# Kernel tuning notes

Measured on AMD Instinct MI355X. Metric: run time of the kernel, lower is better.

## Reference

```python
import jax, jax.numpy as jnp
import numpy as np

B, T, D, C = 16, 2048, 512, 20
K_EASY, K_HARD = 40, 20
M_BIG, M_SMALL = 7, 3
A4 = A5 = A6 = A7 = 1.0
EPS = 1e-05
DROP_P = 0.6


def setup_inputs() -> dict:
    key = jax.random.key(0)
    ks = jax.random.split(key, 6)
    attn = jax.random.uniform(ks[0], (B, T, 1), dtype=jnp.float32)
    mu = jax.random.normal(ks[1], (B, T, D), dtype=jnp.float32)
    var = jax.random.uniform(ks[2], (B, T, D), dtype=jnp.float32) * 0.9 + 0.1
    mu_clip = jax.random.normal(ks[3], (B, T, D), dtype=jnp.float32)
    text_feat = jax.random.normal(ks[4], (C, D), dtype=jnp.float32)
    keep = (jax.random.uniform(ks[5], (B, T)) >= DROP_P).astype(jnp.float32)
    drop_mask = keep / (1.0 - DROP_P)  # inverted-dropout mask on a ones tensor
    return dict(attn=attn, mu=mu, var=var, mu_clip=mu_clip, text_feat=text_feat, drop_mask=drop_mask)


def _normalize(x, axis=-1):
    n = jnp.linalg.norm(x, axis=axis, keepdims=True)
    return x / jnp.maximum(n, 1e-12)


def _select_topk(scores, emb, k):
    # torch: sort desc, take first k indices, gather along time dim
    _, idx = jax.lax.top_k(scores, k)  # [B,k]
    return jnp.take_along_axis(emb, idx[:, :, None], axis=1)  # [B,k,D]


def _window_reduce(x, w, op_min):
    # binary erosion/dilation along time with structure ones((1,w)), border_value=0
    lo, hi = w // 2, w - 1 - w // 2
    xp = jnp.pad(x, ((0, 0), (lo, hi)), constant_values=0.0)
    if op_min:
        return jax.lax.reduce_window(xp, jnp.inf, jax.lax.min, (1, w), (1, 1), 'VALID')
    return jax.lax.reduce_window(xp, -jnp.inf, jax.lax.max, (1, w), (1, 1), 'VALID')


def _kl_distance(mu_p, cov_p, mu_q, cov_q):
    # vectorized over all (i in k_p) x (j in k_q) pairs
    cov_p = cov_p + EPS
    cov_q = cov_q + EPS
    d = mu_p.shape[-1]
    diff = mu_q[:, None, :, :] - mu_p[:, :, None, :]        # [B,kp,kq,D]
    term1 = 0.5 * jnp.sum(diff * diff / cov_q[:, None, :, :], axis=-1)
    term2 = 0.5 * (jnp.sum(jnp.log(cov_q), -1)[:, None, :] - jnp.sum(jnp.log(cov_p), -1)[:, :, None])
    term3 = 0.5 * jnp.sum(cov_p[:, :, None, :] / cov_q[:, None, :, :], axis=-1)
    dist = term1 + term2 + term3 - 0.5 * d
    return jnp.mean(1.0 / (dist + 1.0), axis=(1, 2))        # [B]


def _prob_contrastive(hard_q, easy_pos, easy_neg):
    pos = _kl_distance(hard_q[0], hard_q[1], easy_pos[0], easy_pos[1])
    neg = _kl_distance(hard_q[0], hard_q[1], easy_neg[0], easy_neg[1])
    return jnp.mean(-(jnp.log(pos) + jnp.log(1.0 - neg)))


def _forward(attn, mu, var, mu_clip, text_feat, drop_mask):
    a = attn[..., 0]                                        # [B,T]
    a_drop = a * drop_mask
    a_rev = jnp.max(a, axis=1, keepdims=True) - a
    a_rev_drop = a_rev * drop_mask
    easy_act = (_select_topk(a_drop, mu, K_EASY), _select_topk(a_drop, var, K_EASY))
    easy_bkg = (_select_topk(a_rev_drop, mu, K_EASY), _select_topk(a_rev_drop, var, K_EASY))

    med = jnp.median(a, axis=1, keepdims=True)
    abin = jnp.where(a > med, 1.0, 0.0)
    er_M = _window_reduce(abin, M_BIG, True)
    er_m = _window_reduce(abin, M_SMALL, True)
    inner = jax.lax.stop_gradient(er_m - er_M)              # mask computed on detached numpy in torch
    dl_m = _window_reduce(abin, M_SMALL, False)
    dl_M = _window_reduce(abin, M_BIG, False)
    outer = jax.lax.stop_gradient(dl_M - dl_m)
    a_inner = a * inner
    a_outer = a * outer
    hard_act = (_select_topk(a_inner, mu, K_HARD), _select_topk(a_inner, var, K_HARD))
    hard_bkg = (_select_topk(a_outer, mu, K_HARD), _select_topk(a_outer, var, K_HARD))

    # Distillation
    sim = jnp.einsum('btd,btd->bt', _normalize(mu), _normalize(mu_clip))
    distill = A4 * (-jnp.log(jnp.mean((sim + 1.0) / 2.0)))

    act_loss = A5 * _prob_contrastive(hard_act, easy_act, easy_bkg)
    bkg_loss = A6 * _prob_contrastive(hard_bkg, easy_bkg, easy_act)

    emb = _normalize(text_feat)
    sim_m = emb @ jax.lax.stop_gradient(emb.T) - jnp.eye(emb.shape[0], dtype=emb.dtype)
    ortho = A7 * jnp.linalg.norm(sim_m)

    total = distill + act_loss + bkg_loss + ortho
    return total, distill, act_loss, bkg_loss, ortho


def reference(attn, mu, var, mu_clip, text_feat, drop_mask):
    return _forward(attn, mu, var, mu_clip, text_feat, drop_mask)
```

## Files before the change

### kernel.cpp

```cpp
#include <hip/hip_runtime.h>
#include <math.h>


#define BB 16
#define TT 2048
#define DD 512
#define CC 20
#define KEASY 40
#define KHARD 20
#define EPSF 1e-5f

typedef unsigned long long u64;

template <int CTRL>
__device__ __forceinline__ float dpp_mov(float x) {
  return __int_as_float(__builtin_amdgcn_update_dpp(
      0, __float_as_int(x), CTRL, 0xF, 0xF, true));
}
template <int CTRL, int RM>
__device__ __forceinline__ unsigned dpp_movu(unsigned x) {
  return (unsigned)__builtin_amdgcn_update_dpp(0, (int)x, CTRL, RM, 0xF, true);
}
__device__ __forceinline__ float wsum63(float v) {
  v += dpp_mov<0x111>(v);
  v += dpp_mov<0x112>(v);
  v += dpp_mov<0x114>(v);
  v += dpp_mov<0x118>(v);
  v += dpp_mov<0x142>(v);
  v += dpp_mov<0x143>(v);
  return v;
}
__device__ __forceinline__ float wsum_bc(float v) {
  return __int_as_float(__builtin_amdgcn_readlane(__float_as_int(wsum63(v)), 63));
}
__device__ __forceinline__ float wmax63(float v) {
  v = fmaxf(v, dpp_mov<0x111>(v));
  v = fmaxf(v, dpp_mov<0x112>(v));
  v = fmaxf(v, dpp_mov<0x114>(v));
  v = fmaxf(v, dpp_mov<0x118>(v));
  v = fmaxf(v, dpp_mov<0x142>(v));
  v = fmaxf(v, dpp_mov<0x143>(v));
  return v;
}
__device__ __forceinline__ unsigned wscanu(unsigned v) {
  v += dpp_movu<0x111, 0xF>(v);
  v += dpp_movu<0x112, 0xF>(v);
  v += dpp_movu<0x114, 0xF>(v);
  v += dpp_movu<0x118, 0xF>(v);
  v += dpp_movu<0x142, 0xa>(v);
  v += dpp_movu<0x143, 0xc>(v);
  return v;
}

__device__ __forceinline__ float radix_kth(const float* sbuf, unsigned k,
                                           unsigned* s_hist, unsigned* s_state,
                                           int tid) {
#pragma unroll 1
  for (int round = 0; round < 4; ++round) {
    s_hist[tid] = 0;
    if (round == 0 && tid == 0) { s_state[0] = 0u; s_state[1] = k; }
    __syncthreads();
    const int shift = 24 - 8 * round;
    const unsigned mask_hi = (round == 0) ? 0u : (0xFFFFFFFFu << (shift + 8));
    const unsigned pref = s_state[0];
    const unsigned kk = s_state[1];
    unsigned curbin = 0xFFFFFFFFu, curc = 0;
    for (int i = tid; i < TT; i += 256) {
      const unsigned key = __float_as_uint(sbuf[i]);
      if ((key & mask_hi) == pref) {
        const unsigned bin = 255u - ((key >> shift) & 255u);
        if (bin == curbin) {
          curc++;
        } else {
          if (curc) atomicAdd(&s_hist[curbin], curc);
          curbin = bin;
          curc = 1;
        }
      }
    }
    if (curc) atomicAdd(&s_hist[curbin], curc);
    __syncthreads();
    if (tid < 64) {
      const uint4 h = *(const uint4*)(s_hist + 4 * tid);
      const unsigned s0 = h.x, s1 = s0 + h.y, s2 = s1 + h.z, s3 = s2 + h.w;
      const unsigned P = wscanu(s3);
      const unsigned E = P - s3;
      const u64 bal = __ballot(P >= kk);
      const int L = (int)__ffsll(bal) - 1;
      if (tid == L) {
        unsigned binj, cb;
        if (E + s0 >= kk)      { binj = 0u; cb = E; }
        else if (E + s1 >= kk) { binj = 1u; cb = E + s0; }
        else if (E + s2 >= kk) { binj = 2u; cb = E + s1; }
        else                   { binj = 3u; cb = E + s2; }
        const unsigned digit = 255u - (4u * (unsigned)tid + binj);
        s_state[0] = pref | (digit << shift);
        s_state[1] = kk - cb;
      }
    }
    __syncthreads();
  }
  return __uint_as_float(s_state[0]);
}

__global__ __launch_bounds__(256, 2) void k_main1(const float* __restrict__ attn,
                                                  const float* __restrict__ drop,
                                                  const float* __restrict__ mu,
                                                  const float* __restrict__ muc,
                                                  const float* __restrict__ var,
                                                  int* __restrict__ idxb,
                                                  float* __restrict__ slogb,
                                                  float* __restrict__ part) {
  const int tid = threadIdx.x, wid = tid >> 6, lane = tid & 63;

  if (blockIdx.x >= 64) {
    __shared__ float s_red[4];
    const int blk = blockIdx.x - 64;
    const float* pmu = mu + (size_t)(blk * 4 + wid) * DD + lane * 4;
    const float* pmc = muc + (size_t)(blk * 4 + wid) * DD + lane * 4;
    float4 x[8], y[8];
#pragma unroll
    for (int j = 0; j < 4; j++) {
      const size_t off = (size_t)j * 8192 * DD;
      x[2 * j]     = *(const float4*)(pmu + off);
      x[2 * j + 1] = *(const float4*)(pmu + off + 256);
      y[2 * j]     = *(const float4*)(pmc + off);
      y[2 * j + 1] = *(const float4*)(pmc + off + 256);
    }
    float wacc = 0.f;
#pragma unroll
    for (int j = 0; j < 4; j++) {
      const float4 cxa = x[2 * j], cxb = x[2 * j + 1];
      const float4 cya = y[2 * j], cyb = y[2 * j + 1];
      float dot = 0.f, n1 = 0.f, n2 = 0.f;
      dot = fmaf(cxa.x, cya.x, fmaf(cxa.y, cya.y, fmaf(cxa.z, cya.z, fmaf(cxa.w, cya.w, dot))));
      n1 = fmaf(cxa.x, cxa.x, fmaf(cxa.y, cxa.y, fmaf(cxa.z, cxa.z, fmaf(cxa.w, cxa.w, n1))));
      n2 = fmaf(cya.x, cya.x, fmaf(cya.y, cya.y, fmaf(cya.z, cya.z, fmaf(cya.w, cya.w, n2))));
      dot = fmaf(cxb.x, cyb.x, fmaf(cxb.y, cyb.y, fmaf(cxb.z, cyb.z, fmaf(cxb.w, cyb.w, dot))));
      n1 = fmaf(cxb.x, cxb.x, fmaf(cxb.y, cxb.y, fmaf(cxb.z, cxb.z, fmaf(cxb.w, cxb.w, n1))));
      n2 = fmaf(cyb.x, cyb.x, fmaf(cyb.y, cyb.y, fmaf(cyb.z, cyb.z, fmaf(cyb.w, cyb.w, n2))));
      dot = wsum63(dot);
      n1 = wsum63(n1);
      n2 = wsum63(n2);
      if (lane == 63) {
        const float sim = dot / (fmaxf(sqrtf(n1), 1e-12f) * fmaxf(sqrtf(n2), 1e-12f));
        wacc += (sim + 1.0f) * 0.5f;
      }
    }
    if (lane == 63) s_red[wid] = wacc;
    __syncthreads();
    if (tid == 0) part[blk] = s_red[0] + s_red[1] + s_red[2] + s_red[3];
    return;
  }

  __shared__ float s_a[TT];
  __shared__ float s_v[TT];
  __shared__ __align__(16) unsigned s_hist[256];
  __shared__ unsigned s_state[2];
  __shared__ float s_bc[4];
  __shared__ unsigned s_bcu[4];
  __shared__ int s_idx[KEASY];

  const int b = blockIdx.x >> 2, sel = blockIdx.x & 3;
  for (int i = tid; i < TT; i += 256) s_a[i] = attn[b * TT + i];
  __syncthreads();

  float med = 0.f, mx = 0.f;
  if (sel == 1) {
    float lm = 0.f;
    for (int i = tid; i < TT; i += 256) lm = fmaxf(lm, s_a[i]);
    lm = wmax63(lm);
    if (lane == 63) s_bc[wid] = lm;
    __syncthreads();
    mx = fmaxf(fmaxf(s_bc[0], s_bc[1]), fmaxf(s_bc[2], s_bc[3]));
  } else if (sel >= 2) {
    const float v1 = radix_kth(s_a, 1024u, s_hist, s_state, tid);
    unsigned c = 0;
    float m2 = 0.f;
    for (int i = tid; i < TT; i += 256) {
      const float x = s_a[i];
      c += (x >= v1) ? 1u : 0u;
      m2 = (x < v1) ? fmaxf(m2, x) : m2;
    }
    c = wscanu(c);
    m2 = wmax63(m2);
    if (lane == 63) { s_bc[wid] = m2; s_bcu[wid] = c; }
    __syncthreads();
    const unsigned ctot = s_bcu[0] + s_bcu[1] + s_bcu[2] + s_bcu[3];
    const float m2t = fmaxf(fmaxf(s_bc[0], s_bc[1]), fmaxf(s_bc[2], s_bc[3]));
    const float v2 = (ctot >= 1025u) ? v1 : m2t;
    med = 0.5f * (v1 + v2);
  }

  for (int i = tid; i < TT; i += 256) {
    const float a = s_a[i];
    float score;
    if (sel == 0) {
      score = a * drop[b * TT + i];
    } else if (sel == 1) {
      score = (mx - a) * drop[b * TT + i];
    } else {
      bool sall = true, ball = true, sany = false, bany = false;
#pragma unroll
      for (int o = -3; o <= 3; o++) {
        const int t = i + o;
        const bool one = (t >= 0 && t < TT) ? (s_a[t] > med) : false;
        if (o >= -1 && o <= 1) { sall = sall && one; sany = sany || one; }
        ball = ball && one;
        bany = bany || one;
      }
      score = (sel == 2) ? ((sall && !ball) ? a : 0.f)
                         : ((bany && !sany) ? a : 0.f);
    }
    s_v[i] = score;
  }
  const unsigned K = (sel < 2) ? KEASY : KHARD;
  const float thr = radix_kth(s_v, K, s_hist, s_state, tid);

  if (tid < 64) {
    float v[32];
#pragma unroll
    for (int r = 0; r < 32; r++) v[r] = s_v[r * 64 + lane];
    unsigned cgt = 0;
#pragma unroll
    for (int r = 0; r < 32; r++) cgt += (unsigned)__popcll(__ballot(v[r] > thr));
    unsigned need = (cgt < K) ? (K - cgt) : 0u;
    unsigned base = 0;
    const u64 lmask = (1ull << lane) - 1;
    int* dst = idxb + sel * (BB * KEASY) + b * KEASY;
#pragma unroll
    for (int r = 0; r < 32; r++) {
      const bool gt = v[r] > thr;
      const bool eq = v[r] == thr;
      const u64 beq = __ballot(eq);
      const unsigned neq = (unsigned)__popcll(beq);
      const unsigned take = (need < neq) ? need : neq;
      const bool tk = eq && ((unsigned)__popcll(beq & lmask) < take);
      const u64 bsel = __ballot(gt || tk);
      if (gt || tk) {
        const unsigned pos = base + (unsigned)__popcll(bsel & lmask);
        if (pos < K) {
          dst[pos] = r * 64 + lane;
          s_idx[pos] = r * 64 + lane;
        }
      }
      base += (unsigned)__popcll(bsel);
      need -= take;
    }
  }
  __syncthreads();

  const int Ksel = (sel < 2) ? KEASY : KHARD;
  for (int j = wid; j < Ksel; j += 4) {
    const int t = s_idx[j];
    const float* row = var + ((size_t)b * TT + t) * DD;
    float a2 = 0.f;
#pragma unroll
    for (int c = 0; c < 2; c++) {
      float4 vv = *(const float4*)(row + c * 256 + lane * 4);
      a2 += __logf(vv.x + EPSF) + __logf(vv.y + EPSF) +
            __logf(vv.z + EPSF) + __logf(vv.w + EPSF);
    }
    a2 = wsum63(a2);
    if (lane == 63) slogb[sel * 640 + b * 40 + j] = a2;
  }
}

__global__ __launch_bounds__(256, 1) void k_part2(const float* __restrict__ mu,
                                                  const float* __restrict__ var,
                                                  const int* __restrict__ idxb,
                                                  const float* __restrict__ slogb,
                                                  const float* __restrict__ part,
                                                  const float* __restrict__ text,
                                                  double* __restrict__ acc) {
  __shared__ __align__(16) float smem[2 * KHARD * DD];
  const int tid = threadIdx.x, wid = tid >> 6, lane = tid & 63;
  const int blk = blockIdx.x;

  if (blk < 256) {
    const int b = blk >> 4, klid = (blk >> 2) & 3, qc = blk & 3;
    const int psel = (klid < 2) ? 2 : 3;
    const int qsel = (klid == 0 || klid == 3) ? 0 : 1;
    float* sP1 = smem;
    float* sP2 = smem + KHARD * DD;
    __shared__ float sSlogP[KHARD];
    __shared__ float s_out[4];
    if (tid < KHARD) sSlogP[tid] = slogb[psel * 640 + b * 40 + tid];
    for (int i = tid; i < KHARD * 128; i += 256) {
      const int p = i >> 7, c = (i & 127) * 4;
      const int t = idxb[psel * 640 + b * 40 + p];
      const size_t base = ((size_t)b * TT + t) * DD + c;
      const float4 m = *(const float4*)(mu + base);
      const float4 vv = *(const float4*)(var + base);
      float4 p1;
      p1.x = fmaf(m.x, m.x, vv.x + EPSF);
      p1.y = fmaf(m.y, m.y, vv.y + EPSF);
      p1.z = fmaf(m.z, m.z, vv.z + EPSF);
      p1.w = fmaf(m.w, m.w, vv.w + EPSF);
      *(float4*)(sP1 + p * DD + c) = p1;
      *(float4*)(sP2 + p * DD + c) = m;
    }
    __syncthreads();

    const int d0 = lane * 4, d1 = 256 + lane * 4;
    const int qbase_i = qsel * 640 + b * 40 + qc * 10;
    float wacc = 0.f;
#pragma unroll 1
    for (int j = wid; j < 10; j += 4) {
      const int qidx = idxb[qbase_i + j];
      const float cslq = slogb[qbase_i + j];
      const float* qm = mu + ((size_t)b * TT + qidx) * DD;
      const float* qv = var + ((size_t)b * TT + qidx) * DD;
      const float4 cma = *(const float4*)(qm + d0);
      const float4 cmb = *(const float4*)(qm + d1);
      const float4 cva = *(const float4*)(qv + d0);
      const float4 cvb = *(const float4*)(qv + d1);
      float4 ra, rb, qra, qrb;
      ra.x = 1.0f / (cva.x + EPSF); ra.y = 1.0f / (cva.y + EPSF);
      ra.z = 1.0f / (cva.z + EPSF); ra.w = 1.0f / (cva.w + EPSF);
      rb.x = 1.0f / (cvb.x + EPSF); rb.y = 1.0f / (cvb.y + EPSF);
      rb.z = 1.0f / (cvb.z + EPSF); rb.w = 1.0f / (cvb.w + EPSF);
      qra.x = cma.x * ra.x; qra.y = cma.y * ra.y;
      qra.z = cma.z * ra.z; qra.w = cma.w * ra.w;
      qrb.x = cmb.x * rb.x; qrb.y = cmb.y * rb.y;
      qrb.z = cmb.z * rb.z; qrb.w = cmb.w * rb.w;
      float cqp = cma.x * qra.x + cma.y * qra.y + cma.z * qra.z + cma.w * qra.w +
                  cmb.x * qrb.x + cmb.y * qrb.y + cmb.z * qrb.z + cmb.w * qrb.w;
      const float cq = wsum63(cqp);
      for (int p = 0; p < KHARD; p++) {
        const float4 p1a = *(const float4*)(sP1 + p * DD + d0);
        const float4 p1b = *(const float4*)(sP1 + p * DD + d1);
        const float4 p2a = *(const float4*)(sP2 + p * DD + d0);
        const float4 p2b = *(const float4*)(sP2 + p * DD + d1);
        const float s1 = p1a.x * ra.x + p1a.y * ra.y + p1a.z * ra.z + p1a.w * ra.w +
                         p1b.x * rb.x + p1b.y * rb.y + p1b.z * rb.z + p1b.w * rb.w;
        const float s2 = p2a.x * qra.x + p2a.y * qra.y + p2a.z * qra.z + p2a.w * qra.w +
                         p2b.x * qrb.x + p2b.y * qrb.y + p2b.z * qrb.z + p2b.w * qrb.w;
        const float h = wsum63(fmaf(0.5f, s1, -s2));
        if (lane == 63) {
          const float dist = h + 0.5f * cq + 0.5f * cslq - 0.5f * sSlogP[p] - 256.0f;
          wacc += 1.0f / (dist + 1.0f);
        }
      }
    }
    if (lane == 63) s_out[wid] = wacc;
    __syncthreads();
    if (tid == 0)
      acc[blk] = (double)s_out[0] + s_out[1] + s_out[2] + s_out[3];
    return;
  }

  if (blk == 256) {
    double* sd = (double*)smem;
    double s = 0.0;
    for (int i = tid; i < 2048; i += 256) s += (double)part[i];
    sd[tid] = s;
    __syncthreads();
    for (int st = 128; st; st >>= 1) {
      if (tid < st) sd[tid] += sd[tid + st];
      __syncthreads();
    }
    if (tid == 0) acc[256] = sd[0];
    return;
  }

  {
    float* s_e = smem;
    __shared__ float s_red4[4];
    for (int r = wid; r < CC; r += 4) {
      float4 v[2];
      float ss = 0.f;
#pragma unroll
      for (int c = 0; c < 2; c++) {
        v[c] = *(const float4*)(text + r * DD + c * 256 + lane * 4);
        ss += v[c].x * v[c].x + v[c].y * v[c].y + v[c].z * v[c].z + v[c].w * v[c].w;
      }
      ss = wsum_bc(ss);
      const float n = fmaxf(sqrtf(ss), 1e-12f);
#pragma unroll
      for (int c = 0; c < 2; c++) {
        float4 w = v[c];
        w.x /= n; w.y /= n; w.z /= n; w.w /= n;
        *(float4*)(s_e + r * DD + c * 256 + lane * 4) = w;
      }
    }
    __syncthreads();
    float wss = 0.f;
    for (int p = wid; p < CC * CC; p += 4) {
      const int i = p / CC, j = p % CC;
      float dot = 0.f;
#pragma unroll
      for (int c = 0; c < 2; c++) {
        const int d0 = c * 256 + lane * 4;
        const float4 x = *(const float4*)(s_e + i * DD + d0);
        const float4 y = *(const float4*)(s_e + j * DD + d0);
        dot += x.x * y.x + x.y * y.y + x.z * y.z + x.w * y.w;
      }
      dot = wsum63(dot);
      if (lane == 63) {
        const float s = dot - (i == j ? 1.0f : 0.0f);
        wss += s * s;
      }
    }
    if (lane == 63) s_red4[wid] = wss;
    __syncthreads();
    if (tid == 0)
      acc[257] = (double)(s_red4[0] + s_red4[1] + s_red4[2] + s_red4[3]);
  }
}

__global__ __launch_bounds__(64) void k_final(const double* __restrict__ acc,
                                              float* __restrict__ out) {
  __shared__ double sla[16], slb[16];
  const int tid = threadIdx.x;
  if (tid < 16) {
    const double* ab = acc + tid * 16;
    const double pa = (ab[0] + ab[1] + ab[2] + ab[3]) / 800.0;
    const double na = (ab[4] + ab[5] + ab[6] + ab[7]) / 800.0;
    const double pb = (ab[8] + ab[9] + ab[10] + ab[11]) / 800.0;
    const double nb = (ab[12] + ab[13] + ab[14] + ab[15]) / 800.0;
    sla[tid] = -(log(pa) + log(1.0 - na));
    slb[tid] = -(log(pb) + log(1.0 - nb));
  }
  __syncthreads();
  if (tid == 0) {
    double act = 0.0, bkg = 0.0;
    for (int b = 0; b < 16; b++) { act += sla[b]; bkg += slb[b]; }
    act /= 16.0;
    bkg /= 16.0;
    const double distill = -log(acc[256] / (double)(BB * TT));
    const double ortho = sqrt(acc[257]);
    const double total = distill + act + bkg + ortho;
    out[0] = (float)total;
    out[1] = (float)distill;
    out[2] = (float)act;
    out[3] = (float)bkg;
    out[4] = (float)ortho;
  }
}

extern "C" void kernel_launch(void* const* d_in, const int* in_sizes, int n_in,
                              void* d_out, int out_size, void* d_ws, size_t ws_size,
                              hipStream_t stream) {
  const float* attn = (const float*)d_in[0];
  const float* mu   = (const float*)d_in[1];
  const float* var  = (const float*)d_in[2];
  const float* muc  = (const float*)d_in[3];
  const float* text = (const float*)d_in[4];
  const float* drop = (const float*)d_in[5];
  float* out = (float*)d_out;

  double* acc  = (double*)d_ws;
  int* idxb    = (int*)(acc + 258);
  float* slogb = (float*)(idxb + 2560);
  float* part  = (float*)(slogb + 2560);

  k_main1<<<2112, 256, 0, stream>>>(attn, drop, mu, muc, var, idxb, slogb, part);
  k_part2<<<258, 256, 0, stream>>>(mu, var, idxb, slogb, part, text, acc);
  k_final<<<1, 64, 0, stream>>>(acc, out);
}
```

Baseline: 240.9 us.

## Split top-k selection into its own kernel, merge distill with KL stage

Moves the 64 top-k selection blocks into a small first kernel and packs the 2048 distillation blocks into the second kernel alongside the KL and ortho blocks, so the bandwidth-heavy cosine-similarity pass overlaps with the pairwise-KL work rather than with selection. The part-sum reduction moves into the final kernel. Radix-select histograms become per-wave copies to cut shared-memory atomic contention. The trade-off is that the KL blocks can no longer overlap with selection, and the second kernel carries larger shared memory for every block, including the distill blocks.

```diff
diff --git a/kernel.cpp b/kernel.cpp
--- a/kernel.cpp
+++ b/kernel.cpp
@@ -53,17 +53,21 @@
 }
 
 __device__ __forceinline__ float radix_kth(const float* sbuf, unsigned k,
-                                           unsigned* s_hist, unsigned* s_state,
-                                           int tid) {
+                                           unsigned* s_hist4, unsigned* s_state,
+                                           int tid, int wid) {
 #pragma unroll 1
   for (int round = 0; round < 4; ++round) {
-    s_hist[tid] = 0;
+    s_hist4[tid] = 0;
+    s_hist4[256 + tid] = 0;
+    s_hist4[512 + tid] = 0;
+    s_hist4[768 + tid] = 0;
     if (round == 0 && tid == 0) { s_state[0] = 0u; s_state[1] = k; }
     __syncthreads();
     const int shift = 24 - 8 * round;
     const unsigned mask_hi = (round == 0) ? 0u : (0xFFFFFFFFu << (shift + 8));
     const unsigned pref = s_state[0];
     const unsigned kk = s_state[1];
+    unsigned* myhist = s_hist4 + (wid << 8);
     unsigned curbin = 0xFFFFFFFFu, curc = 0;
     for (int i = tid; i < TT; i += 256) {
       const unsigned key = __float_as_uint(sbuf[i]);
@@ -72,17 +76,24 @@
         if (bin == curbin) {
           curc++;
         } else {
-          if (curc) atomicAdd(&s_hist[curbin], curc);
+          if (curc) atomicAdd(&myhist[curbin], curc);
           curbin = bin;
           curc = 1;
         }
       }
     }
-    if (curc) atomicAdd(&s_hist[curbin], curc);
+    if (curc) atomicAdd(&myhist[curbin], curc);
     __syncthreads();
     if (tid < 64) {
-      const uint4 h = *(const uint4*)(s_hist + 4 * tid);
-      const unsigned s0 = h.x, s1 = s0 + h.y, s2 = s1 + h.z, s3 = s2 + h.w;
+      const uint4 h0 = *(const uint4*)(s_hist4 + 4 * tid);
+      const uint4 h1 = *(const uint4*)(s_hist4 + 256 + 4 * tid);
+      const uint4 h2 = *(const uint4*)(s_hist4 + 512 + 4 * tid);
+      const uint4 h3 = *(const uint4*)(s_hist4 + 768 + 4 * tid);
+      const unsigned b0 = h0.x + h1.x + h2.x + h3.x;
+      const unsigned b1 = h0.y + h1.y + h2.y + h3.y;
+      const unsigned b2 = h0.z + h1.z + h2.z + h3.z;
+      const unsigned b3 = h0.w + h1.w + h2.w + h3.w;
+      const unsigned s0 = b0, s1 = s0 + b1, s2 = s1 + b2, s3 = s2 + b3;
       const unsigned P = wscanu(s3);
       const unsigned E = P - s3;
       const u64 bal = __ballot(P >= kk);
@@ -103,21 +114,142 @@
   return __uint_as_float(s_state[0]);
 }
 
-__global__ __launch_bounds__(256, 2) void k_main1(const float* __restrict__ attn,
-                                                  const float* __restrict__ drop,
-                                                  const float* __restrict__ mu,
+__global__ __launch_bounds__(256, 2) void k_sel(const float* __restrict__ attn,
+                                                const float* __restrict__ drop,
+                                                const float* __restrict__ var,
+                                                int* __restrict__ idxb,
+                                                float* __restrict__ slogb) {
+  const int tid = threadIdx.x, wid = tid >> 6, lane = tid & 63;
+  __shared__ float s_a[TT];
+  __shared__ float s_v[TT];
+  __shared__ __align__(16) unsigned s_hist4[1024];
+  __shared__ unsigned s_state[2];
+  __shared__ float s_bc[4];
+  __shared__ unsigned s_bcu[4];
+  __shared__ int s_idx[KEASY];
+
+  const int b = blockIdx.x >> 2, sel = blockIdx.x & 3;
+  for (int i = tid; i < TT; i += 256) s_a[i] = attn[b * TT + i];
+  __syncthreads();
+
+  float med = 0.f, mx = 0.f;
+  if (sel == 1) {
+    float lm = 0.f;
+    for (int i = tid; i < TT; i += 256) lm = fmaxf(lm, s_a[i]);
+    lm = wmax63(lm);
+    if (lane == 63) s_bc[wid] = lm;
+    __syncthreads();
+    mx = fmaxf(fmaxf(s_bc[0], s_bc[1]), fmaxf(s_bc[2], s_bc[3]));
+  } else if (sel >= 2) {
+    const float v1 = radix_kth(s_a, 1024u, s_hist4, s_state, tid, wid);
+    unsigned c = 0;
+    float m2 = 0.f;
+    for (int i = tid; i < TT; i += 256) {
+      const float x = s_a[i];
+      c += (x >= v1) ? 1u : 0u;
+      m2 = (x < v1) ? fmaxf(m2, x) : m2;
+    }
+    c = wscanu(c);
+    m2 = wmax63(m2);
+    if (lane == 63) { s_bc[wid] = m2; s_bcu[wid] = c; }
+    __syncthreads();
+    const unsigned ctot = s_bcu[0] + s_bcu[1] + s_bcu[2] + s_bcu[3];
+    const float m2t = fmaxf(fmaxf(s_bc[0], s_bc[1]), fmaxf(s_bc[2], s_bc[3]));
+    const float v2 = (ctot >= 1025u) ? v1 : m2t;
+    med = 0.5f * (v1 + v2);
+  }
+
+  for (int i = tid; i < TT; i += 256) {
+    const float a = s_a[i];
+    float score;
+    if (sel == 0) {
+      score = a * drop[b * TT + i];
+    } else if (sel == 1) {
+      score = (mx - a) * drop[b * TT + i];
+    } else {
+      bool sall = true, ball = true, sany = false, bany = false;
+#pragma unroll
+      for (int o = -3; o <= 3; o++) {
+        const int t = i + o;
+        const bool one = (t >= 0 && t < TT) ? (s_a[t] > med) : false;
+        if (o >= -1 && o <= 1) { sall = sall && one; sany = sany || one; }
+        ball = ball && one;
+        bany = bany || one;
+      }
+      score = (sel == 2) ? ((sall && !ball) ? a : 0.f)
+                         : ((bany && !sany) ? a : 0.f);
+    }
+    s_v[i] = score;
+  }
+  const unsigned K = (sel < 2) ? KEASY : KHARD;
+  const float thr = radix_kth(s_v, K, s_hist4, s_state, tid, wid);
+
+  if (tid < 64) {
+    float v[32];
+#pragma unroll
+    for (int r = 0; r < 32; r++) v[r] = s_v[r * 64 + lane];
+    unsigned cgt = 0;
+#pragma unroll
+    for (int r = 0; r < 32; r++) cgt += (unsigned)__popcll(__ballot(v[r] > thr));
+    unsigned need = (cgt < K) ? (K - cgt) : 0u;
+    unsigned base = 0;
+    const u64 lmask = (1ull << lane) - 1;
+    int* dst = idxb + sel * (BB * KEASY) + b * KEASY;
+#pragma unroll
+    for (int r = 0; r < 32; r++) {
+      const bool gt = v[r] > thr;
+      const bool eq = v[r] == thr;
+      const u64 beq = __ballot(eq);
+      const unsigned neq = (unsigned)__popcll(beq);
+      const unsigned take = (need < neq) ? need : neq;
+      const bool tk = eq && ((unsigned)__popcll(beq & lmask) < take);
+      const u64 bsel = __ballot(gt || tk);
+      if (gt || tk) {
+        const unsigned pos = base + (unsigned)__popcll(bsel & lmask);
+        if (pos < K) {
+          dst[pos] = r * 64 + lane;
+          s_idx[pos] = r * 64 + lane;
+        }
+      }
+      base += (unsigned)__popcll(bsel);
+      need -= take;
+    }
+  }
+  __syncthreads();
+
+  const int Ksel = (sel < 2) ? KEASY : KHARD;
+  for (int j = wid; j < Ksel; j += 4) {
+    const int t = s_idx[j];
+    const float* row = var + ((size_t)b * TT + t) * DD;
+    float a2 = 0.f;
+#pragma unroll
+    for (int c = 0; c < 2; c++) {
+      float4 vv = *(const float4*)(row + c * 256 + lane * 4);
+      a2 += __logf(vv.x + EPSF) + __logf(vv.y + EPSF) +
+            __logf(vv.z + EPSF) + __logf(vv.w + EPSF);
+    }
+    a2 = wsum63(a2);
+    if (lane == 63) slogb[sel * 640 + b * 40 + j] = a2;
+  }
+}
+
+__global__ __launch_bounds__(256, 2) void k_main2(const float* __restrict__ mu,
+                                                  const float* __restrict__ var,
                                                   const float* __restrict__ muc,
-                                                  const float* __restrict__ var,
-                                                  int* __restrict__ idxb,
-                                                  float* __restrict__ slogb,
+                                                  const int* __restrict__ idxb,
+                                                  const float* __restrict__ slogb,
+                                                  const float* __restrict__ text,
+                                                  double* __restrict__ acc,
                                                   float* __restrict__ part) {
+  __shared__ __align__(16) float smem[2 * KHARD * DD];
   const int tid = threadIdx.x, wid = tid >> 6, lane = tid & 63;
-
-  if (blockIdx.x >= 64) {
-    __shared__ float s_red[4];
-    const int blk = blockIdx.x - 64;
-    const float* pmu = mu + (size_t)(blk * 4 + wid) * DD + lane * 4;
-    const float* pmc = muc + (size_t)(blk * 4 + wid) * DD + lane * 4;
+  const int blk = blockIdx.x;
+
+  if (blk >= 257) {
+    float* s_red = smem;
+    const int dblk = blk - 257;
+    const float* pmu = mu + (size_t)(dblk * 4 + wid) * DD + lane * 4;
+    const float* pmc = muc + (size_t)(dblk * 4 + wid) * DD + lane * 4;
     float4 x[8], y[8];
 #pragma unroll
     for (int j = 0; j < 4; j++) {
@@ -149,133 +281,9 @@
     }
     if (lane == 63) s_red[wid] = wacc;
     __syncthreads();
-    if (tid == 0) part[blk] = s_red[0] + s_red[1] + s_red[2] + s_red[3];
+    if (tid == 0) part[dblk] = s_red[0] + s_red[1] + s_red[2] + s_red[3];
     return;
   }
-
-  __shared__ float s_a[TT];
-  __shared__ float s_v[TT];
-  __shared__ __align__(16) unsigned s_hist[256];
-  __shared__ unsigned s_state[2];
-  __shared__ float s_bc[4];
-  __shared__ unsigned s_bcu[4];
-  __shared__ int s_idx[KEASY];
-
-  const int b = blockIdx.x >> 2, sel = blockIdx.x & 3;
-  for (int i = tid; i < TT; i += 256) s_a[i] = attn[b * TT + i];
-  __syncthreads();
-
-  float med = 0.f, mx = 0.f;
-  if (sel == 1) {
-    float lm = 0.f;
-    for (int i = tid; i < TT; i += 256) lm = fmaxf(lm, s_a[i]);
-    lm = wmax63(lm);
-    if (lane == 63) s_bc[wid] = lm;
-    __syncthreads();
-    mx = fmaxf(fmaxf(s_bc[0], s_bc[1]), fmaxf(s_bc[2], s_bc[3]));
-  } else if (sel >= 2) {
-    const float v1 = radix_kth(s_a, 1024u, s_hist, s_state, tid);
-    unsigned c = 0;
-    float m2 = 0.f;
-    for (int i = tid; i < TT; i += 256) {
-      const float x = s_a[i];
-      c += (x >= v1) ? 1u : 0u;
-      m2 = (x < v1) ? fmaxf(m2, x) : m2;
-    }
-    c = wscanu(c);
-    m2 = wmax63(m2);
-    if (lane == 63) { s_bc[wid] = m2; s_bcu[wid] = c; }
-    __syncthreads();
-    const unsigned ctot = s_bcu[0] + s_bcu[1] + s_bcu[2] + s_bcu[3];
-    const float m2t = fmaxf(fmaxf(s_bc[0], s_bc[1]), fmaxf(s_bc[2], s_bc[3]));
-    const float v2 = (ctot >= 1025u) ? v1 : m2t;
-    med = 0.5f * (v1 + v2);
-  }
-
-  for (int i = tid; i < TT; i += 256) {
-    const float a = s_a[i];
-    float score;
-    if (sel == 0) {
-      score = a * drop[b * TT + i];
-    } else if (sel == 1) {
-      score = (mx - a) * drop[b * TT + i];
-    } else {
-      bool sall = true, ball = true, sany = false, bany = false;
-#pragma unroll
-      for (int o = -3; o <= 3; o++) {
-        const int t = i + o;
-        const bool one = (t >= 0 && t < TT) ? (s_a[t] > med) : false;
-        if (o >= -1 && o <= 1) { sall = sall && one; sany = sany || one; }
-        ball = ball && one;
-        bany = bany || one;
-      }
-      score = (sel == 2) ? ((sall && !ball) ? a : 0.f)
-                         : ((bany && !sany) ? a : 0.f);
-    }
-    s_v[i] = score;
-  }
-  const unsigned K = (sel < 2) ? KEASY : KHARD;
-  const float thr = radix_kth(s_v, K, s_hist, s_state, tid);
-
-  if (tid < 64) {
-    float v[32];
-#pragma unroll
-    for (int r = 0; r < 32; r++) v[r] = s_v[r * 64 + lane];
-    unsigned cgt = 0;
-#pragma unroll
-    for (int r = 0; r < 32; r++) cgt += (unsigned)__popcll(__ballot(v[r] > thr));
-    unsigned need = (cgt < K) ? (K - cgt) : 0u;
-    unsigned base = 0;
-    const u64 lmask = (1ull << lane) - 1;
-    int* dst = idxb + sel * (BB * KEASY) + b * KEASY;
-#pragma unroll
-    for (int r = 0; r < 32; r++) {
-      const bool gt = v[r] > thr;
-      const bool eq = v[r] == thr;
-      const u64 beq = __ballot(eq);
-      const unsigned neq = (unsigned)__popcll(beq);
-      const unsigned take = (need < neq) ? need : neq;
-      const bool tk = eq && ((unsigned)__popcll(beq & lmask) < take);
-      const u64 bsel = __ballot(gt || tk);
-      if (gt || tk) {
-        const unsigned pos = base + (unsigned)__popcll(bsel & lmask);
-        if (pos < K) {
-          dst[pos] = r * 64 + lane;
-          s_idx[pos] = r * 64 + lane;
-        }
-      }
-      base += (unsigned)__popcll(bsel);
-      need -= take;
-    }
-  }
-  __syncthreads();
-
-  const int Ksel = (sel < 2) ? KEASY : KHARD;
-  for (int j = wid; j < Ksel; j += 4) {
-    const int t = s_idx[j];
-    const float* row = var + ((size_t)b * TT + t) * DD;
-    float a2 = 0.f;
-#pragma unroll
-    for (int c = 0; c < 2; c++) {
-      float4 vv = *(const float4*)(row + c * 256 + lane * 4);
-      a2 += __logf(vv.x + EPSF) + __logf(vv.y + EPSF) +
-            __logf(vv.z + EPSF) + __logf(vv.w + EPSF);
-    }
-    a2 = wsum63(a2);
-    if (lane == 63) slogb[sel * 640 + b * 40 + j] = a2;
-  }
-}
-
-__global__ __launch_bounds__(256, 1) void k_part2(const float* __restrict__ mu,
-                                                  const float* __restrict__ var,
-                                                  const int* __restrict__ idxb,
-                                                  const float* __restrict__ slogb,
-                                                  const float* __restrict__ part,
-                                                  const float* __restrict__ text,
-                                                  double* __restrict__ acc) {
-  __shared__ __align__(16) float smem[2 * KHARD * DD];
-  const int tid = threadIdx.x, wid = tid >> 6, lane = tid & 63;
-  const int blk = blockIdx.x;
 
   if (blk < 256) {
     const int b = blk >> 4, klid = (blk >> 2) & 3, qc = blk & 3;
@@ -350,20 +358,6 @@
     return;
   }
 
-  if (blk == 256) {
-    double* sd = (double*)smem;
-    double s = 0.0;
-    for (int i = tid; i < 2048; i += 256) s += (double)part[i];
-    sd[tid] = s;
-    __syncthreads();
-    for (int st = 128; st; st >>= 1) {
-      if (tid < st) sd[tid] += sd[tid + st];
-      __syncthreads();
-    }
-    if (tid == 0) acc[256] = sd[0];
-    return;
-  }
-
   {
     float* s_e = smem;
     __shared__ float s_red4[4];
@@ -405,14 +399,24 @@
     if (lane == 63) s_red4[wid] = wss;
     __syncthreads();
     if (tid == 0)
-      acc[257] = (double)(s_red4[0] + s_red4[1] + s_red4[2] + s_red4[3]);
-  }
-}
-
-__global__ __launch_bounds__(64) void k_final(const double* __restrict__ acc,
-                                              float* __restrict__ out) {
+      acc[256] = (double)(s_red4[0] + s_red4[1] + s_red4[2] + s_red4[3]);
+  }
+}
+
+__global__ __launch_bounds__(256) void k_final(const double* __restrict__ acc,
+                                               const float* __restrict__ part,
+                                               float* __restrict__ out) {
+  __shared__ double sd[256];
   __shared__ double sla[16], slb[16];
   const int tid = threadIdx.x;
+  double s = 0.0;
+  for (int i = tid; i < 2048; i += 256) s += (double)part[i];
+  sd[tid] = s;
+  __syncthreads();
+  for (int st = 128; st; st >>= 1) {
+    if (tid < st) sd[tid] += sd[tid + st];
+    __syncthreads();
+  }
   if (tid < 16) {
     const double* ab = acc + tid * 16;
     const double pa = (ab[0] + ab[1] + ab[2] + ab[3]) / 800.0;
@@ -428,8 +432,8 @@
     for (int b = 0; b < 16; b++) { act += sla[b]; bkg += slb[b]; }
     act /= 16.0;
     bkg /= 16.0;
-    const double distill = -log(acc[256] / (double)(BB * TT));
-    const double ortho = sqrt(acc[257]);
+    const double distill = -log(sd[0] / (double)(BB * TT));
+    const double ortho = sqrt(acc[256]);
     const double total = distill + act + bkg + ortho;
     out[0] = (float)total;
     out[1] = (float)distill;
@@ -451,11 +455,11 @@
   float* out = (float*)d_out;
 
   double* acc  = (double*)d_ws;
-  int* idxb    = (int*)(acc + 258);
+  int* idxb    = (int*)(acc + 257);
   float* slogb = (float*)(idxb + 2560);
   float* part  = (float*)(slogb + 2560);
 
-  k_main1<<<2112, 256, 0, stream>>>(attn, drop, mu, muc, var, idxb, slogb, part);
-  k_part2<<<258, 256, 0, stream>>>(mu, var, idxb, slogb, part, text, acc);
-  k_final<<<1, 64, 0, stream>>>(acc, out);
-}
+  k_sel<<<64, 256, 0, stream>>>(attn, drop, var, idxb, slogb);
+  k_main2<<<2305, 256, 0, stream>>>(mu, var, muc, idxb, slogb, text, acc, part);
+  k_final<<<1, 256, 0, stream>>>(acc, part, out);
+}
```

Result: faster. 235.9 us (-2.1%).
